# Kernel optimization log

Measured on AMD Instinct MI355X. Metric: run time of the kernel, lower is better.

## Reference

```python
import jax, jax.numpy as jnp
import numpy as np

B, Q, C, H = 4, 256, 1024, 128
NEG_SLOPE = 0.01  # F.leaky_relu default


def setup_inputs() -> dict:
    key = jax.random.key(0)
    ks = jax.random.split(key, 6)
    return {
        "query": jax.random.normal(ks[0], (B, Q, H), dtype=jnp.float32),
        "context": jax.random.normal(ks[1], (B, C, H), dtype=jnp.float32),
        "Ww": jax.random.normal(ks[2], (H, 2 * H), dtype=jnp.float32) * 0.05,
        "bw": jax.random.normal(ks[3], (H,), dtype=jnp.float32) * 0.05,
        "Ws": jax.random.normal(ks[4], (1, H), dtype=jnp.float32) * 0.05,
        "bs": jax.random.normal(ks[5], (1,), dtype=jnp.float32) * 0.05,
    }


def reference(query, context, Ww, bw, Ws, bs):
    # Faithful to: leaky_relu(Linear(cat(q_expand, c_expand))) then score, softmax, bmm.
    # cat+linear is split into per-input projections (mathematically identical),
    # avoiding the (B,Q,C,2H) concat materialization.
    h = query.shape[-1]
    Wq, Wc = Ww[:, :h], Ww[:, h:]
    hq = jnp.einsum('bqh,kh->bqk', query, Wq)            # (B,Q,H)
    hc = jnp.einsum('bch,kh->bck', context, Wc) + bw     # (B,C,H)
    hidden = jax.nn.leaky_relu(hq[:, :, None, :] + hc[:, None, :, :], NEG_SLOPE)  # (B,Q,C,H)
    score = jnp.einsum('bqch,oh->bqc', hidden, Ws) + bs[0]  # (B,Q,C)
    attn = jax.nn.softmax(score, axis=-1)                   # (B,Q,C)
    attn_output = jnp.einsum('bqc,bch->bqh', attn, context)  # mix=True bmm
    return (attn_output, attn)
```

## Files before the change

### kernel.cpp

```cpp
#include <hip/hip_runtime.h>

#define B_   4
#define Q_   256
#define C_   1024
#define H_   128
#define NEG  0.01f

__global__ __launch_bounds__(128) void proj_kernel(
    const float* __restrict__ query, const float* __restrict__ context,
    const float* __restrict__ Ww, const float* __restrict__ bw,
    float* __restrict__ hq, float* __restrict__ hc)
{
    const int blk = blockIdx.x;
    const int k = threadIdx.x;
    const bool is_q = (blk < (B_ * Q_ / 8));
    const int row0 = is_q ? (blk * 8) : ((blk - B_ * Q_ / 8) * 8);
    const float* __restrict__ in = is_q ? query : context;
    float* __restrict__ out = is_q ? hq : hc;

    const float4* __restrict__ Wrow =
        reinterpret_cast<const float4*>(Ww + k * (2 * H_) + (is_q ? 0 : H_));
    const float4* __restrict__ in4 =
        reinterpret_cast<const float4*>(in + row0 * H_);

    float acc[8] = {0.f, 0.f, 0.f, 0.f, 0.f, 0.f, 0.f, 0.f};
    #pragma unroll 8
    for (int h4 = 0; h4 < H_ / 4; ++h4) {
        const float4 wvv = Wrow[h4];
        #pragma unroll
        for (int r = 0; r < 8; ++r) {
            const float4 iv = in4[r * (H_ / 4) + h4];
            acc[r] += iv.x * wvv.x + iv.y * wvv.y + iv.z * wvv.z + iv.w * wvv.w;
        }
    }
    const float bias = is_q ? 0.f : bw[k];
    #pragma unroll
    for (int r = 0; r < 8; ++r)
        out[(row0 + r) * H_ + k] = acc[r] + bias;
}

__global__ __launch_bounds__(512) void attn_kernel(
    const float* __restrict__ hq, const float* __restrict__ hc,
    const float* __restrict__ Ws, const float* __restrict__ context,
    float* __restrict__ outA, float* __restrict__ outP)
{
    const int b  = blockIdx.x >> 6;
    const int q0 = (blockIdx.x & 63) * 4;
    const int t  = threadIdx.x;
    const int wv = t >> 6;

    __shared__ float4 attn4_s[C_];
    __shared__ float  red[16 * 4 * H_];
    __shared__ float  wred[8][4];
    __shared__ float  wsum[8][4];

    const float4* __restrict__ hq4  = reinterpret_cast<const float4*>(hq);
    const float4* __restrict__ hc4  = reinterpret_cast<const float4*>(hc);
    const float4* __restrict__ ws4  = reinterpret_cast<const float4*>(Ws);
    const float4* __restrict__ ctx4 = reinterpret_cast<const float4*>(context);

    float s[4][2] = {{0.f,0.f},{0.f,0.f},{0.f,0.f},{0.f,0.f}};
    const int c0 = t, c1 = t + 512;
    #pragma unroll 4
    for (int k0 = 0; k0 < H_ / 4; ++k0) {
        const float4 wsv = ws4[k0];
        float4 hqv[4];
        #pragma unroll
        for (int q = 0; q < 4; ++q)
            hqv[q] = hq4[(b * Q_ + q0 + q) * (H_ / 4) + k0];
        #pragma unroll
        for (int ci = 0; ci < 2; ++ci) {
            const int c = ci ? c1 : c0;
            const float4 hcv = hc4[(b * C_ + c) * (H_ / 4) + k0];
            #pragma unroll
            for (int q = 0; q < 4; ++q) {
                float x0 = hqv[q].x + hcv.x;
                float x1 = hqv[q].y + hcv.y;
                float x2 = hqv[q].z + hcv.z;
                float x3 = hqv[q].w + hcv.w;
                x0 = fmaxf(x0, NEG * x0);
                x1 = fmaxf(x1, NEG * x1);
                x2 = fmaxf(x2, NEG * x2);
                x3 = fmaxf(x3, NEG * x3);
                s[q][ci] += wsv.x * x0 + wsv.y * x1 + wsv.z * x2 + wsv.w * x3;
            }
        }
    }

    float m[4];
    #pragma unroll
    for (int q = 0; q < 4; ++q) {
        float v = fmaxf(s[q][0], s[q][1]);
        #pragma unroll
        for (int off = 32; off >= 1; off >>= 1)
            v = fmaxf(v, __shfl_xor(v, off, 64));
        m[q] = v;
    }
    if ((t & 63) == 0) {
        #pragma unroll
        for (int q = 0; q < 4; ++q) wred[wv][q] = m[q];
    }
    __syncthreads();
    #pragma unroll
    for (int q = 0; q < 4; ++q) {
        float v = wred[0][q];
        #pragma unroll
        for (int i = 1; i < 8; ++i) v = fmaxf(v, wred[i][q]);
        m[q] = v;
    }
    float e[4][2], p[4];
    #pragma unroll
    for (int q = 0; q < 4; ++q) {
        e[q][0] = __expf(s[q][0] - m[q]);
        e[q][1] = __expf(s[q][1] - m[q]);
        float v = e[q][0] + e[q][1];
        #pragma unroll
        for (int off = 32; off >= 1; off >>= 1)
            v += __shfl_xor(v, off, 64);
        p[q] = v;
    }
    if ((t & 63) == 0) {
        #pragma unroll
        for (int q = 0; q < 4; ++q) wsum[wv][q] = p[q];
    }
    __syncthreads();
    float rS[4];
    #pragma unroll
    for (int q = 0; q < 4; ++q) {
        float S = wsum[0][q];
        #pragma unroll
        for (int i = 1; i < 8; ++i) S += wsum[i][q];
        rS[q] = 1.0f / S;
    }
    float a0[4], a1[4];
    #pragma unroll
    for (int q = 0; q < 4; ++q) {
        a0[q] = e[q][0] * rS[q];
        a1[q] = e[q][1] * rS[q];
    }
    attn4_s[c0] = make_float4(a0[0], a0[1], a0[2], a0[3]);
    attn4_s[c1] = make_float4(a1[0], a1[1], a1[2], a1[3]);
    #pragma unroll
    for (int q = 0; q < 4; ++q) {
        outP[(b * Q_ + q0 + q) * C_ + c0] = a0[q];
        outP[(b * Q_ + q0 + q) * C_ + c1] = a1[q];
    }
    __syncthreads();

    const int hg   = t & 31;
    const int crep = t >> 5;
    float4 acc[4] = {{0,0,0,0},{0,0,0,0},{0,0,0,0},{0,0,0,0}};
    const int cb = crep * 64;
    #pragma unroll 4
    for (int cc = 0; cc < 64; ++cc) {
        const int c = cb + cc;
        const float4 a4 = attn4_s[c];
        const float4 xv = ctx4[(b * C_ + c) * (H_ / 4) + hg];
        acc[0].x += a4.x * xv.x; acc[0].y += a4.x * xv.y; acc[0].z += a4.x * xv.z; acc[0].w += a4.x * xv.w;
        acc[1].x += a4.y * xv.x; acc[1].y += a4.y * xv.y; acc[1].z += a4.y * xv.z; acc[1].w += a4.y * xv.w;
        acc[2].x += a4.z * xv.x; acc[2].y += a4.z * xv.y; acc[2].z += a4.z * xv.z; acc[2].w += a4.z * xv.w;
        acc[3].x += a4.w * xv.x; acc[3].y += a4.w * xv.y; acc[3].z += a4.w * xv.z; acc[3].w += a4.w * xv.w;
    }
    float4* red4 = reinterpret_cast<float4*>(red);
    #pragma unroll
    for (int q = 0; q < 4; ++q)
        red4[(crep * 4 + q) * 32 + hg] = acc[q];
    __syncthreads();
    {
        const int q = t >> 7, h = t & 127;
        float v = 0.f;
        #pragma unroll
        for (int cr = 0; cr < 16; ++cr)
            v += red[(cr * 4 + q) * H_ + h];
        outA[(b * Q_ + q0 + q) * H_ + h] = v;
    }
}

extern "C" void kernel_launch(void* const* d_in, const int* in_sizes, int n_in,
                              void* d_out, int out_size, void* d_ws, size_t ws_size,
                              hipStream_t stream) {
    const float* query   = (const float*)d_in[0];
    const float* context = (const float*)d_in[1];
    const float* Ww      = (const float*)d_in[2];
    const float* bw      = (const float*)d_in[3];
    const float* Ws      = (const float*)d_in[4];

    float* outA = (float*)d_out;
    float* outP = outA + B_ * Q_ * H_;

    float* hq = (float*)d_ws;
    float* hc = hq + B_ * Q_ * H_;

    hipLaunchKernelGGL(proj_kernel, dim3(640), dim3(128), 0, stream,
                       query, context, Ww, bw, hq, hc);
    hipLaunchKernelGGL(attn_kernel, dim3(256), dim3(512), 0, stream,
                       hq, hc, Ws, context, outA, outP);
}
```

Before: 110.2 us.

## Rewrite leaky-relu scoring via abs identity and stage hq/Ws in LDS

Measured after the change: 102.3 us, median of 2. 7.2% less time.

```diff
diff --git a/kernel.cpp b/kernel.cpp
--- a/kernel.cpp
+++ b/kernel.cpp
@@ -13,8 +13,8 @@
 {
     const int blk = blockIdx.x;
     const int k = threadIdx.x;
-    const bool is_q = (blk < (B_ * Q_ / 8));
-    const int row0 = is_q ? (blk * 8) : ((blk - B_ * Q_ / 8) * 8);
+    const bool is_q = (blk < (B_ * Q_ / 4));
+    const int row0 = is_q ? (blk * 4) : ((blk - B_ * Q_ / 4) * 4);
     const float* __restrict__ in = is_q ? query : context;
     float* __restrict__ out = is_q ? hq : hc;
 
@@ -23,19 +23,19 @@
     const float4* __restrict__ in4 =
         reinterpret_cast<const float4*>(in + row0 * H_);
 
-    float acc[8] = {0.f, 0.f, 0.f, 0.f, 0.f, 0.f, 0.f, 0.f};
-    #pragma unroll 8
+    float acc[4] = {0.f, 0.f, 0.f, 0.f};
+    #pragma unroll 4
     for (int h4 = 0; h4 < H_ / 4; ++h4) {
-        const float4 wvv = Wrow[h4];
-        #pragma unroll
-        for (int r = 0; r < 8; ++r) {
+        const float4 w = Wrow[h4];
+        #pragma unroll
+        for (int r = 0; r < 4; ++r) {
             const float4 iv = in4[r * (H_ / 4) + h4];
-            acc[r] += iv.x * wvv.x + iv.y * wvv.y + iv.z * wvv.z + iv.w * wvv.w;
+            acc[r] += iv.x * w.x + iv.y * w.y + iv.z * w.z + iv.w * w.w;
         }
     }
     const float bias = is_q ? 0.f : bw[k];
     #pragma unroll
-    for (int r = 0; r < 8; ++r)
+    for (int r = 0; r < 4; ++r)
         out[(row0 + r) * H_ + k] = acc[r] + bias;
 }
 
@@ -44,47 +44,82 @@
     const float* __restrict__ Ws, const float* __restrict__ context,
     float* __restrict__ outA, float* __restrict__ outP)
 {
-    const int b  = blockIdx.x >> 6;
-    const int q0 = (blockIdx.x & 63) * 4;
+    const int b  = blockIdx.x & 3;
+    const int q0 = (blockIdx.x >> 2) * 4;
     const int t  = threadIdx.x;
     const int wv = t >> 6;
 
     __shared__ float4 attn4_s[C_];
     __shared__ float  red[16 * 4 * H_];
+    __shared__ float  s_hq[4][H_];
+    __shared__ float  s_ws[H_];
     __shared__ float  wred[8][4];
     __shared__ float  wsum[8][4];
-
-    const float4* __restrict__ hq4  = reinterpret_cast<const float4*>(hq);
-    const float4* __restrict__ hc4  = reinterpret_cast<const float4*>(hc);
-    const float4* __restrict__ ws4  = reinterpret_cast<const float4*>(Ws);
-    const float4* __restrict__ ctx4 = reinterpret_cast<const float4*>(context);
-
-    float s[4][2] = {{0.f,0.f},{0.f,0.f},{0.f,0.f},{0.f,0.f}};
+    __shared__ float  dqp[2][4];
+
+    {
+        const int q = t >> 7, k = t & 127;
+        s_hq[q][k] = hq[(b * Q_ + q0 + q) * H_ + k];
+        if (t < H_) s_ws[t] = Ws[t];
+    }
+    __syncthreads();
+
+    if (t < 128) {
+        float v[4];
+        #pragma unroll
+        for (int q = 0; q < 4; ++q) v[q] = s_ws[t] * s_hq[q][t];
+        #pragma unroll
+        for (int off = 32; off >= 1; off >>= 1) {
+            #pragma unroll
+            for (int q = 0; q < 4; ++q) v[q] += __shfl_xor(v[q], off, 64);
+        }
+        if ((t & 63) == 0) {
+            #pragma unroll
+            for (int q = 0; q < 4; ++q) dqp[t >> 6][q] = v[q];
+        }
+    }
+    __syncthreads();
+    float Dq[4];
+    #pragma unroll
+    for (int q = 0; q < 4; ++q) Dq[q] = dqp[0][q] + dqp[1][q];
+
     const int c0 = t, c1 = t + 512;
+    const float4* __restrict__ ws4 = reinterpret_cast<const float4*>(s_ws);
+    const float4* __restrict__ hcp0 =
+        reinterpret_cast<const float4*>(hc + (b * C_ + c0) * H_);
+    const float4* __restrict__ hcp1 =
+        reinterpret_cast<const float4*>(hc + (b * C_ + c1) * H_);
+
+    float sabs[4][2] = {{0.f,0.f},{0.f,0.f},{0.f,0.f},{0.f,0.f}};
+    float dc0 = 0.f, dc1 = 0.f;
     #pragma unroll 4
     for (int k0 = 0; k0 < H_ / 4; ++k0) {
         const float4 wsv = ws4[k0];
         float4 hqv[4];
         #pragma unroll
         for (int q = 0; q < 4; ++q)
-            hqv[q] = hq4[(b * Q_ + q0 + q) * (H_ / 4) + k0];
-        #pragma unroll
-        for (int ci = 0; ci < 2; ++ci) {
-            const int c = ci ? c1 : c0;
-            const float4 hcv = hc4[(b * C_ + c) * (H_ / 4) + k0];
-            #pragma unroll
-            for (int q = 0; q < 4; ++q) {
-                float x0 = hqv[q].x + hcv.x;
-                float x1 = hqv[q].y + hcv.y;
-                float x2 = hqv[q].z + hcv.z;
-                float x3 = hqv[q].w + hcv.w;
-                x0 = fmaxf(x0, NEG * x0);
-                x1 = fmaxf(x1, NEG * x1);
-                x2 = fmaxf(x2, NEG * x2);
-                x3 = fmaxf(x3, NEG * x3);
-                s[q][ci] += wsv.x * x0 + wsv.y * x1 + wsv.z * x2 + wsv.w * x3;
-            }
-        }
+            hqv[q] = reinterpret_cast<const float4*>(s_hq[q])[k0];
+        const float4 h0 = hcp0[k0];
+        const float4 h1 = hcp1[k0];
+        dc0 += wsv.x * h0.x + wsv.y * h0.y + wsv.z * h0.z + wsv.w * h0.w;
+        dc1 += wsv.x * h1.x + wsv.y * h1.y + wsv.z * h1.z + wsv.w * h1.w;
+        #pragma unroll
+        for (int q = 0; q < 4; ++q) {
+            sabs[q][0] += wsv.x * fabsf(hqv[q].x + h0.x)
+                        + wsv.y * fabsf(hqv[q].y + h0.y)
+                        + wsv.z * fabsf(hqv[q].z + h0.z)
+                        + wsv.w * fabsf(hqv[q].w + h0.w);
+            sabs[q][1] += wsv.x * fabsf(hqv[q].x + h1.x)
+                        + wsv.y * fabsf(hqv[q].y + h1.y)
+                        + wsv.z * fabsf(hqv[q].z + h1.z)
+                        + wsv.w * fabsf(hqv[q].w + h1.w);
+        }
+    }
+    float s[4][2];
+    #pragma unroll
+    for (int q = 0; q < 4; ++q) {
+        s[q][0] = 0.505f * (Dq[q] + dc0) + 0.495f * sabs[q][0];
+        s[q][1] = 0.505f * (Dq[q] + dc1) + 0.495f * sabs[q][1];
     }
 
     float m[4];
@@ -147,6 +182,7 @@
     }
     __syncthreads();
 
+    const float4* __restrict__ ctx4 = reinterpret_cast<const float4*>(context);
     const int hg   = t & 31;
     const int crep = t >> 5;
     float4 acc[4] = {{0,0,0,0},{0,0,0,0},{0,0,0,0},{0,0,0,0}};
@@ -191,7 +227,7 @@
     float* hq = (float*)d_ws;
     float* hc = hq + B_ * Q_ * H_;
 
-    hipLaunchKernelGGL(proj_kernel, dim3(640), dim3(128), 0, stream,
+    hipLaunchKernelGGL(proj_kernel, dim3(1280), dim3(128), 0, stream,
                        query, context, Ww, bw, hq, hc);
     hipLaunchKernelGGL(attn_kernel, dim3(256), dim3(512), 0, stream,
                        hq, hc, Ws, context, outA, outP);
```
